# Performance work log

Measured on AMD Instinct MI355X. Metric: run time of the kernel, lower is better.

The kernel has to match this reference:

```python
import jax, jax.numpy as jnp
import numpy as np

THETA = 10000.0
N_HEADS = 16


def setup_inputs() -> dict:
    key = jax.random.key(0)
    kx, kq, kk, kv, ko = jax.random.split(key, 5)
    B, S, D = 2, 2048, 1024
    std = np.sqrt(2.0 / (D + D))
    def mk_w(k):
        # trunc_normal in [-3*std, 3*std], stored as [in_features, out_features]
        return jax.random.truncated_normal(k, -3.0, 3.0, (D, D), jnp.float32) * std
    return {
        "x": jax.random.normal(kx, (B, S, D), dtype=jnp.float32),
        "token_positions": jnp.arange(S, dtype=jnp.int64) if jax.config.jax_enable_x64 else jnp.arange(S, dtype=jnp.int32),
        "WQ": mk_w(kq),
        "WK": mk_w(kk),
        "WV": mk_w(kv),
        "WO": mk_w(ko),
    }


def _rope(x, pos, theta):
    # x: [B, H, S, d_k]; pos: [S]
    d_k = x.shape[-1]
    freq = 1.0 / theta ** (jnp.arange(0, d_k, 2, dtype=jnp.float32) / d_k)  # [d_k//2]
    ang = pos.astype(jnp.float32)[:, None] * freq                            # [S, d_k//2]
    cos, sin = jnp.cos(ang), jnp.sin(ang)
    xp = x.reshape(x.shape[:-1] + (d_k // 2, 2))
    x0, x1 = xp[..., 0], xp[..., 1]
    r0 = cos * x0 - sin * x1
    r1 = sin * x0 + cos * x1
    return jnp.stack([r0, r1], axis=-1).reshape(x.shape)


def reference(x, token_positions, WQ, WK, WV, WO):
    B, S, D = x.shape
    H = N_HEADS
    dk = D // H
    # Linear in source computes y = x @ W.T (W stored [in, out], used transposed)
    def proj(W):
        return jnp.einsum('oi,bsi->bso', W, x).reshape(B, S, H, dk).transpose(0, 2, 1, 3)
    Q = proj(WQ)  # [B, H, S, dk]
    K = proj(WK)
    V = proj(WV)
    Q = _rope(Q, token_positions, THETA)
    K = _rope(K, token_positions, THETA)
    scores = jnp.einsum('bhqd,bhkd->bhqk', Q, K) / np.sqrt(dk).astype(np.float32)
    causal = jnp.tril(jnp.ones((S, S), dtype=bool))
    scores = jnp.where(causal, scores, jnp.float32(-1e9))
    w = jax.nn.softmax(scores, axis=-1)
    out = jnp.einsum('bhqk,bhkd->bhqd', w, V)
    out = out.transpose(0, 2, 1, 3).reshape(B, S, D)
    return jnp.einsum('oi,bsi->bso', WO, out)
```

## Files before the change

kernel.cpp:

```cpp
#include <hip/hip_runtime.h>
#include <hip/hip_bf16.h>

#define S_LEN   2048
#define D_MODEL 1024
#define NH      16
#define DKH     64
#define BATCH   2
#define BS_ROWS 4096

typedef unsigned short u16;
typedef unsigned int   u32;
typedef __attribute__((ext_vector_type(4)))  float f32x4;
typedef __attribute__((ext_vector_type(16))) float f32x16;
typedef __attribute__((ext_vector_type(8)))  short bf16x8;

__device__ __forceinline__ float bf2f(u16 u) {
  union { unsigned int i; float f; } v; v.i = ((unsigned int)u) << 16; return v.f;
}
__device__ __forceinline__ u16 f2bf(float f) {
  union { __hip_bfloat16 h; u16 u; } cv; cv.h = __float2bfloat16(f); return cv.u;
}
__device__ __forceinline__ u32 pkbf(float a, float b) {
  return (u32)f2bf(a) | ((u32)f2bf(b) << 16);
}
__device__ __forceinline__ f32x4 mfma16(bf16x8 a, bf16x8 b, f32x4 c) {
  return __builtin_amdgcn_mfma_f32_16x16x32_bf16(a, b, c, 0, 0, 0);
}
__device__ __forceinline__ f32x16 mfma32(bf16x8 a, bf16x8 b, f32x16 c) {
  return __builtin_amdgcn_mfma_f32_32x32x16_bf16(a, b, c, 0, 0, 0);
}
__device__ __forceinline__ void gl_lds16(const u16* g, u16* l) {
  __builtin_amdgcn_global_load_lds(
      (const __attribute__((address_space(1))) void*)g,
      (__attribute__((address_space(3))) void*)l, 16, 0, 0);
}

__global__ void cvt_all(const float* __restrict__ x,
                        const float* __restrict__ wq, const float* __restrict__ wk,
                        const float* __restrict__ wv, const float* __restrict__ wo,
                        u16* __restrict__ xb, u16* __restrict__ wqb, u16* __restrict__ wkb,
                        u16* __restrict__ wvb, u16* __restrict__ wob) {
  int seg = blockIdx.y;
  const float* src; u16* dst;
  if (seg < 4)      { src = x + (size_t)seg * (1u << 20); dst = xb + (size_t)seg * (1u << 20); }
  else if (seg == 4){ src = wq; dst = wqb; }
  else if (seg == 5){ src = wk; dst = wkb; }
  else if (seg == 6){ src = wv; dst = wvb; }
  else              { src = wo; dst = wob; }
  int i = blockIdx.x * 256 + threadIdx.x;
  float4 v = reinterpret_cast<const float4*>(src)[i];
  ushort4 o;
  o.x = f2bf(v.x); o.y = f2bf(v.y); o.z = f2bf(v.z); o.w = f2bf(v.w);
  reinterpret_cast<ushort4*>(dst)[i] = o;
}

#define BM 128
#define BN 128
#define BKK 64

__global__ __launch_bounds__(256) void gemm_bt(
    const u16* __restrict__ A,
    const u16* __restrict__ B0, const u16* __restrict__ B1, const u16* __restrict__ B2,
    u16* __restrict__ C0, u16* __restrict__ C1, u16* __restrict__ C2,
    float* __restrict__ Cf,
    int M, int N, int K, int out_f32)
{
  __shared__ __align__(16) u16 As[BM * BKK];
  __shared__ __align__(16) u16 Bs[BN * BKK];

  const int z = blockIdx.z;
  const u16* Bm = (z == 0) ? B0 : ((z == 1) ? B1 : B2);
  u16* Cb = (z == 0) ? C0 : ((z == 1) ? C1 : C2);

  const int tid = threadIdx.x;
  const int l = tid & 63, w = tid >> 6;
  const int lr = l & 15, lg = l >> 4;
  const int m0 = blockIdx.y * BM, n0 = blockIdx.x * BN;
  const int wr = w >> 1, wc = w & 1;

  f32x4 acc[4][4];
#pragma unroll
  for (int mi = 0; mi < 4; ++mi)
#pragma unroll
    for (int nj = 0; nj < 4; ++nj)
      acc[mi][nj] = (f32x4){0.f, 0.f, 0.f, 0.f};

  for (int k0 = 0; k0 < K; k0 += BKK) {
    __syncthreads();
#pragma unroll
    for (int i = 0; i < 4; ++i) {
      int Dc = w * 256 + i * 64 + l;
      int row = Dc >> 3;
      int c = (Dc & 7) ^ (row & 7);
      gl_lds16(A  + (size_t)(m0 + row) * K + k0 + c * 8, As + (w * 256 + i * 64) * 8);
      gl_lds16(Bm + (size_t)(n0 + row) * K + k0 + c * 8, Bs + (w * 256 + i * 64) * 8);
    }
    __syncthreads();

    bf16x8 af[2][4], bfr[2][4];
#pragma unroll
    for (int kk = 0; kk < 2; ++kk)
#pragma unroll
      for (int mi = 0; mi < 4; ++mi) {
        int rowa = wr * 64 + mi * 16 + lr;
        int ck = kk * 4 + lg;
        af[kk][mi] = *(const bf16x8*)&As[rowa * BKK + (((ck) ^ (rowa & 7)) << 3)];
        int rowb = wc * 64 + mi * 16 + lr;
        bfr[kk][mi] = *(const bf16x8*)&Bs[rowb * BKK + (((ck) ^ (rowb & 7)) << 3)];
      }
#pragma unroll
    for (int kk = 0; kk < 2; ++kk)
#pragma unroll
      for (int mi = 0; mi < 4; ++mi)
#pragma unroll
        for (int nj = 0; nj < 4; ++nj)
          acc[mi][nj] = mfma16(af[kk][mi], bfr[kk][nj], acc[mi][nj]);
  }

#pragma unroll
  for (int mi = 0; mi < 4; ++mi)
#pragma unroll
    for (int nj = 0; nj < 4; ++nj)
#pragma unroll
      for (int r = 0; r < 4; ++r) {
        int row = m0 + wr * 64 + mi * 16 + lg * 4 + r;
        int col = n0 + wc * 64 + nj * 16 + lr;
        float v = acc[mi][nj][r];
        if (out_f32) Cf[(size_t)row * N + col] = v;
        else         Cb[(size_t)row * N + col] = f2bf(v);
      }
}

__global__ void rope_pack(const u16* __restrict__ Yq, const u16* __restrict__ Yk,
                          const int* __restrict__ pos,
                          u16* __restrict__ Qb, u16* __restrict__ Kb)
{
  int t = blockIdx.x * blockDim.x + threadIdx.x;
  if (t >= BS_ROWS * (D_MODEL / 2)) return;
  int pi = t & 511;
  int r  = t >> 9;
  int h = pi >> 5, j = pi & 31;
  int b = r >> 11, s = r & (S_LEN - 1);
  int p = pos[s];

  float freq = exp2f(-(float)j * 0.41524101186092028f);
  float ang = (float)p * freq;
  float sn, cs;
  sincosf(ang, &sn, &cs);

  int base = r * D_MODEL + pi * 2;
  float q0 = bf2f(Yq[base]), q1 = bf2f(Yq[base + 1]);
  float k0 = bf2f(Yk[base]), k1 = bf2f(Yk[base + 1]);

  const float QS = 0.18033688011112042f;
  float qr0 = (cs * q0 - sn * q1) * QS;
  float qr1 = (sn * q0 + cs * q1) * QS;
  float kr0 = cs * k0 - sn * k1;
  float kr1 = sn * k0 + cs * k1;

  int bh = b * NH + h;
  size_t qidx = ((size_t)bh * S_LEN + s) * DKH + 2 * j;
  ushort2 qo; qo.x = f2bf(qr0); qo.y = f2bf(qr1);
  ushort2 ko; ko.x = f2bf(kr0); ko.y = f2bf(kr1);
  *reinterpret_cast<ushort2*>(Qb + qidx) = qo;
  *reinterpret_cast<ushort2*>(Kb + qidx) = ko;
}

__global__ __launch_bounds__(256) void transpose_v(const u16* __restrict__ Yv,
                                                   u16* __restrict__ Vt)
{
  __shared__ u32 T[64][65];
  const int sb = blockIdx.x;
  const int bh = blockIdx.y;
  const int b = bh >> 4, h = bh & 15;
  const int t = threadIdx.x;
  const int s0 = sb * 64;

#pragma unroll
  for (int pass = 0; pass < 2; ++pass) {
    int row = pass * 32 + (t >> 3);
    int c0 = (t & 7) * 8;
    bf16x8 v = *(const bf16x8*)(Yv + (size_t)(b * S_LEN + s0 + row) * D_MODEL + h * DKH + c0);
#pragma unroll
    for (int i = 0; i < 8; ++i) T[row][c0 + i] = (u32)(u16)v[i];
  }
  __syncthreads();

  const int d = t >> 2, ch = t & 3;
  bf16x8 o0, o1;
#pragma unroll
  for (int i = 0; i < 8; ++i) o0[i] = (short)(u16)T[ch * 16 + i][d];
#pragma unroll
  for (int i = 0; i < 8; ++i) o1[i] = (short)(u16)T[ch * 16 + 8 + i][d];
  u16* dst = Vt + ((size_t)bh * DKH + d) * S_LEN + s0 + ch * 16;
  *(bf16x8*)dst = o0;
  *(bf16x8*)(dst + 8) = o1;
}

__global__ __launch_bounds__(256, 2) void attn_fwd(
    const u16* __restrict__ Qb, const u16* __restrict__ Kb,
    const u16* __restrict__ Vt, u16* __restrict__ Ob)
{
  const int f = blockIdx.x;
  const int qt = (f < 256) ? (f >> 5) : (23 - (f >> 5));
  const int bh = f & 31;
  const int b = bh >> 4, h = bh & 15;
  const int tid = threadIdx.x, l = tid & 63, w = tid >> 6;
  const int lq = l & 31;
  const int hi = l >> 5;

  __shared__ __align__(16) u16 Ks[2][64 * 64];
  __shared__ __align__(16) u16 Vs[2][64 * 64];

  const u16* Qh = Qb + (size_t)bh * S_LEN * DKH;
  const u16* Kh = Kb + (size_t)bh * S_LEN * DKH;
  const u16* Vh = Vt + (size_t)bh * DKH * S_LEN;

  const int q0w = qt * 128 + w * 32;
  const int qg  = q0w + lq;

  bf16x8 qf[4];
#pragma unroll
  for (int ks = 0; ks < 4; ++ks)
    qf[ks] = *(const bf16x8*)(Qh + (size_t)qg * DKH + ks * 16 + hi * 8);

  f32x16 oacc[2];
#pragma unroll
  for (int r = 0; r < 16; ++r) { oacc[0][r] = 0.f; oacc[1][r] = 0.f; }
  float m = -INFINITY, lsum = 0.f;

#define STAGE(buf, tt) do {                                                        \
    int kv0s = (tt) * 64;                                                          \
    _Pragma("unroll")                                                              \
    for (int i = 0; i < 2; ++i) {                                                  \
      int Dc = w * 128 + i * 64 + l;                                               \
      int row = Dc >> 3;                                                           \
      int c = (Dc & 7) ^ (row & 7);                                                \
      gl_lds16(Kh + (size_t)(kv0s + row) * DKH + c * 8, &Ks[buf][(w * 128 + i * 64) * 8]); \
      gl_lds16(Vh + (size_t)row * S_LEN + kv0s + c * 8, &Vs[buf][(w * 128 + i * 64) * 8]); \
    }                                                                              \
  } while (0)

  const int nt = 2 * qt + 2;
  STAGE(0, 0);
  __syncthreads();
  int cur = 0;
  for (int t = 0; t < nt; ++t) {
    if (t + 1 < nt) STAGE(cur ^ 1, t + 1);
    const int kv0 = t * 64;
    if (kv0 <= q0w + 31) {
      f32x16 sv0, sv1;
#pragma unroll
      for (int r = 0; r < 16; ++r) { sv0[r] = 0.f; sv1[r] = 0.f; }
#pragma unroll
      for (int ks = 0; ks < 4; ++ks) {
        int c0 = ((ks * 2 + hi) ^ (l & 7)) << 3;
        bf16x8 k0 = *(const bf16x8*)&Ks[cur][lq * 64 + c0];
        bf16x8 k1 = *(const bf16x8*)&Ks[cur][(32 + lq) * 64 + c0];
        sv0 = mfma32(k0, qf[ks], sv0);
        sv1 = mfma32(k1, qf[ks], sv1);
      }
      if (kv0 + 63 > q0w) {
#pragma unroll
        for (int r = 0; r < 16; ++r) {
          int kvl = (r & 3) + 8 * (r >> 2) + 4 * hi;
          if (kv0 + kvl > qg)      sv0[r] = -1e30f;
          if (kv0 + 32 + kvl > qg) sv1[r] = -1e30f;
        }
      }
      float pm = sv0[0];
#pragma unroll
      for (int r = 1; r < 16; ++r) pm = fmaxf(pm, sv0[r]);
#pragma unroll
      for (int r = 0; r < 16; ++r) pm = fmaxf(pm, sv1[r]);
      pm = fmaxf(pm, __shfl_xor(pm, 32));
      if (__any(pm > m + 8.f)) {
        float mn = fmaxf(m, pm);
        float sc = exp2f(m - mn);
        m = mn; lsum *= sc;
#pragma unroll
        for (int r = 0; r < 16; ++r) {
          float sr = __shfl(sc, (r & 3) + 8 * (r >> 2) + 4 * hi);
          oacc[0][r] *= sr; oacc[1][r] *= sr;
        }
      }
      float ps = 0.f;
#pragma unroll
      for (int r = 0; r < 16; ++r) { float p = exp2f(sv0[r] - m); sv0[r] = p; ps += p; }
#pragma unroll
      for (int r = 0; r < 16; ++r) { float p = exp2f(sv1[r] - m); sv1[r] = p; ps += p; }
      lsum += ps;
#pragma unroll
      for (int s = 0; s < 2; ++s) {
        u32 w0[4], w1[4];
#pragma unroll
        for (int g = 0; g < 4; ++g) {
          float a0 = s ? sv1[4 * g]     : sv0[4 * g];
          float a1 = s ? sv1[4 * g + 1] : sv0[4 * g + 1];
          float a2 = s ? sv1[4 * g + 2] : sv0[4 * g + 2];
          float a3 = s ? sv1[4 * g + 3] : sv0[4 * g + 3];
          w0[g] = pkbf(a0, a1);
          w1[g] = pkbf(a2, a3);
        }
#pragma unroll
        for (int t2 = 0; t2 < 2; ++t2) {
          u32 xo0 = hi ? w0[2 * t2 + 1] : w0[2 * t2];
          u32 xo1 = hi ? w1[2 * t2 + 1] : w1[2 * t2];
          u32 sp0 = hi ? w0[2 * t2]     : w0[2 * t2 + 1];
          u32 sp1 = hi ? w1[2 * t2]     : w1[2 * t2 + 1];
          u32 yo0 = __shfl_xor(sp0, 32);
          u32 yo1 = __shfl_xor(sp1, 32);
          union { u32 u[4]; bf16x8 v; } pa;
          pa.u[0] = hi ? yo0 : xo0;
          pa.u[1] = hi ? yo1 : xo1;
          pa.u[2] = hi ? xo0 : yo0;
          pa.u[3] = hi ? xo1 : yo1;
          int ks2 = s * 2 + t2;
          int cv = ((ks2 * 2 + hi) ^ (l & 7)) << 3;
#pragma unroll
          for (int dh = 0; dh < 2; ++dh) {
            bf16x8 vf = *(const bf16x8*)&Vs[cur][(dh * 32 + lq) * 64 + cv];
            oacc[dh] = mfma32(pa.v, vf, oacc[dh]);
          }
        }
      }
    }
    __syncthreads();
    cur ^= 1;
  }
#undef STAGE

  float ltot = lsum + __shfl_xor(lsum, 32);
  float inv = 1.0f / ltot;
  u16* obase = Ob + (size_t)b * S_LEN * D_MODEL + (size_t)h * DKH;
#pragma unroll
  for (int r = 0; r < 16; ++r) {
    int ql = (r & 3) + 8 * (r >> 2) + 4 * hi;
    float ir = __shfl(inv, ql);
    u16* orow = obase + (size_t)(q0w + ql) * D_MODEL;
    orow[lq]      = f2bf(oacc[0][r] * ir);
    orow[32 + lq] = f2bf(oacc[1][r] * ir);
  }
}

extern "C" void kernel_launch(void* const* d_in, const int* in_sizes, int n_in,
                              void* d_out, int out_size, void* d_ws, size_t ws_size,
                              hipStream_t stream) {
  const float* x   = (const float*)d_in[0];
  const int*   pos = (const int*)d_in[1];
  const float* WQ  = (const float*)d_in[2];
  const float* WK  = (const float*)d_in[3];
  const float* WV  = (const float*)d_in[4];
  const float* WO  = (const float*)d_in[5];

  char* ws = (char*)d_ws;
  u16* xb  = (u16*)(ws);
  u16* wqb = (u16*)(ws + (size_t)(8)  * 1048576);
  u16* wkb = (u16*)(ws + (size_t)(10) * 1048576);
  u16* wvb = (u16*)(ws + (size_t)(12) * 1048576);
  u16* wob = (u16*)(ws + (size_t)(14) * 1048576);
  u16* Yq  = (u16*)(ws + (size_t)(16) * 1048576);
  u16* Yk  = (u16*)(ws + (size_t)(24) * 1048576);
  u16* Yv  = (u16*)(ws + (size_t)(32) * 1048576);
  u16* Qb  = (u16*)(ws + (size_t)(40) * 1048576);
  u16* Kb  = (u16*)(ws + (size_t)(48) * 1048576);
  u16* Vt  = (u16*)(ws + (size_t)(56) * 1048576);
  u16* Ob  = (u16*)(ws + (size_t)(64) * 1048576);

  cvt_all<<<dim3(1024, 8), 256, 0, stream>>>(x, WQ, WK, WV, WO, xb, wqb, wkb, wvb, wob);

  gemm_bt<<<dim3(D_MODEL / BN, BS_ROWS / BM, 3), 256, 0, stream>>>(
      xb, wqb, wkb, wvb, Yq, Yk, Yv, nullptr, BS_ROWS, D_MODEL, D_MODEL, 0);

  rope_pack<<<(BS_ROWS * (D_MODEL / 2)) / 256, 256, 0, stream>>>(
      Yq, Yk, pos, Qb, Kb);

  transpose_v<<<dim3(S_LEN / 64, BATCH * NH), 256, 0, stream>>>(Yv, Vt);

  attn_fwd<<<dim3(512), 256, 0, stream>>>(Qb, Kb, Vt, Ob);

  gemm_bt<<<dim3(D_MODEL / BN, BS_ROWS / BM, 1), 256, 0, stream>>>(
      Ob, wob, wob, wob, nullptr, nullptr, nullptr, (float*)d_out,
      BS_ROWS, D_MODEL, D_MODEL, 1);
}
```

Measured before the change: 226.9 us.

## Restructure attention into single-wave blocks with 32-row KV tiles

The attention kernel moves from 256-thread blocks handling 128 query rows to 64-thread single-wave blocks handling 32 query rows, launched as 2048 blocks in longest-first order. KV tiles shrink to 32 rows with their own swizzle, the causal masking becomes exact per tile, and __syncthreads is replaced by a vmcnt wait because only one wave touches shared memory. The aim is finer-grained parallelism, better load balance across the causal triangle and no block-level barriers. In exchange, each block reuses K/V less, so global/L2 traffic for K and V grows, and each wave does more loads per MFMA.

```diff
diff --git a/kernel.cpp b/kernel.cpp
--- a/kernel.cpp
+++ b/kernel.cpp
@@ -197,138 +197,132 @@
   *(bf16x8*)(dst + 8) = o1;
 }
 
-__global__ __launch_bounds__(256, 2) void attn_fwd(
+__global__ __launch_bounds__(64) void attn_fwd(
     const u16* __restrict__ Qb, const u16* __restrict__ Kb,
     const u16* __restrict__ Vt, u16* __restrict__ Ob)
 {
   const int f = blockIdx.x;
-  const int qt = (f < 256) ? (f >> 5) : (23 - (f >> 5));
+  const int qt = 63 - (f >> 5);
   const int bh = f & 31;
   const int b = bh >> 4, h = bh & 15;
-  const int tid = threadIdx.x, l = tid & 63, w = tid >> 6;
-  const int lq = l & 31;
-  const int hi = l >> 5;
-
-  __shared__ __align__(16) u16 Ks[2][64 * 64];
-  __shared__ __align__(16) u16 Vs[2][64 * 64];
+  const int l = threadIdx.x & 63;
+  const int lq = l & 31, hi = l >> 5;
+
+  __shared__ __align__(16) u16 Ks[2][32 * 64];
+  __shared__ __align__(16) u16 Vs[2][64 * 32];
 
   const u16* Qh = Qb + (size_t)bh * S_LEN * DKH;
   const u16* Kh = Kb + (size_t)bh * S_LEN * DKH;
   const u16* Vh = Vt + (size_t)bh * DKH * S_LEN;
 
-  const int q0w = qt * 128 + w * 32;
-  const int qg  = q0w + lq;
+  const int q0 = qt * 32;
 
   bf16x8 qf[4];
 #pragma unroll
   for (int ks = 0; ks < 4; ++ks)
-    qf[ks] = *(const bf16x8*)(Qh + (size_t)qg * DKH + ks * 16 + hi * 8);
+    qf[ks] = *(const bf16x8*)(Qh + (size_t)(q0 + lq) * DKH + ks * 16 + hi * 8);
+
+  const u16* ksrc[4];
+  const u16* vsrc[4];
+#pragma unroll
+  for (int i = 0; i < 4; ++i) {
+    int Dc = i * 64 + l;
+    int row = Dc >> 3;
+    int c = (Dc & 7) ^ (row & 7);
+    ksrc[i] = Kh + (size_t)row * DKH + c * 8;
+  }
+#pragma unroll
+  for (int i = 0; i < 4; ++i) {
+    int Dc = i * 64 + l;
+    int d = Dc >> 2;
+    int c = (Dc & 3) ^ (d & 3);
+    vsrc[i] = Vh + (size_t)d * S_LEN + c * 8;
+  }
 
   f32x16 oacc[2];
 #pragma unroll
   for (int r = 0; r < 16; ++r) { oacc[0][r] = 0.f; oacc[1][r] = 0.f; }
   float m = -INFINITY, lsum = 0.f;
 
-#define STAGE(buf, tt) do {                                                        \
-    int kv0s = (tt) * 64;                                                          \
-    _Pragma("unroll")                                                              \
-    for (int i = 0; i < 2; ++i) {                                                  \
-      int Dc = w * 128 + i * 64 + l;                                               \
-      int row = Dc >> 3;                                                           \
-      int c = (Dc & 7) ^ (row & 7);                                                \
-      gl_lds16(Kh + (size_t)(kv0s + row) * DKH + c * 8, &Ks[buf][(w * 128 + i * 64) * 8]); \
-      gl_lds16(Vh + (size_t)row * S_LEN + kv0s + c * 8, &Vs[buf][(w * 128 + i * 64) * 8]); \
-    }                                                                              \
-  } while (0)
-
-  const int nt = 2 * qt + 2;
-  STAGE(0, 0);
-  __syncthreads();
+  auto stage = [&](int buf, int t) {
+    const size_t koff = (size_t)t * 32 * DKH;
+    const size_t voff = (size_t)t * 32;
+#pragma unroll
+    for (int i = 0; i < 4; ++i) gl_lds16(ksrc[i] + koff, &Ks[buf][i * 512]);
+#pragma unroll
+    for (int i = 0; i < 4; ++i) gl_lds16(vsrc[i] + voff, &Vs[buf][i * 512]);
+  };
+
+  const int nt = qt + 1;
+  stage(0, 0);
   int cur = 0;
   for (int t = 0; t < nt; ++t) {
-    if (t + 1 < nt) STAGE(cur ^ 1, t + 1);
-    const int kv0 = t * 64;
-    if (kv0 <= q0w + 31) {
-      f32x16 sv0, sv1;
-#pragma unroll
-      for (int r = 0; r < 16; ++r) { sv0[r] = 0.f; sv1[r] = 0.f; }
-#pragma unroll
-      for (int ks = 0; ks < 4; ++ks) {
-        int c0 = ((ks * 2 + hi) ^ (l & 7)) << 3;
-        bf16x8 k0 = *(const bf16x8*)&Ks[cur][lq * 64 + c0];
-        bf16x8 k1 = *(const bf16x8*)&Ks[cur][(32 + lq) * 64 + c0];
-        sv0 = mfma32(k0, qf[ks], sv0);
-        sv1 = mfma32(k1, qf[ks], sv1);
-      }
-      if (kv0 + 63 > q0w) {
-#pragma unroll
-        for (int r = 0; r < 16; ++r) {
-          int kvl = (r & 3) + 8 * (r >> 2) + 4 * hi;
-          if (kv0 + kvl > qg)      sv0[r] = -1e30f;
-          if (kv0 + 32 + kvl > qg) sv1[r] = -1e30f;
-        }
-      }
-      float pm = sv0[0];
-#pragma unroll
-      for (int r = 1; r < 16; ++r) pm = fmaxf(pm, sv0[r]);
-#pragma unroll
-      for (int r = 0; r < 16; ++r) pm = fmaxf(pm, sv1[r]);
-      pm = fmaxf(pm, __shfl_xor(pm, 32));
-      if (__any(pm > m + 8.f)) {
-        float mn = fmaxf(m, pm);
-        float sc = exp2f(m - mn);
-        m = mn; lsum *= sc;
-#pragma unroll
-        for (int r = 0; r < 16; ++r) {
-          float sr = __shfl(sc, (r & 3) + 8 * (r >> 2) + 4 * hi);
-          oacc[0][r] *= sr; oacc[1][r] *= sr;
-        }
-      }
-      float ps = 0.f;
-#pragma unroll
-      for (int r = 0; r < 16; ++r) { float p = exp2f(sv0[r] - m); sv0[r] = p; ps += p; }
-#pragma unroll
-      for (int r = 0; r < 16; ++r) { float p = exp2f(sv1[r] - m); sv1[r] = p; ps += p; }
-      lsum += ps;
-#pragma unroll
-      for (int s = 0; s < 2; ++s) {
-        u32 w0[4], w1[4];
-#pragma unroll
-        for (int g = 0; g < 4; ++g) {
-          float a0 = s ? sv1[4 * g]     : sv0[4 * g];
-          float a1 = s ? sv1[4 * g + 1] : sv0[4 * g + 1];
-          float a2 = s ? sv1[4 * g + 2] : sv0[4 * g + 2];
-          float a3 = s ? sv1[4 * g + 3] : sv0[4 * g + 3];
-          w0[g] = pkbf(a0, a1);
-          w1[g] = pkbf(a2, a3);
-        }
-#pragma unroll
-        for (int t2 = 0; t2 < 2; ++t2) {
-          u32 xo0 = hi ? w0[2 * t2 + 1] : w0[2 * t2];
-          u32 xo1 = hi ? w1[2 * t2 + 1] : w1[2 * t2];
-          u32 sp0 = hi ? w0[2 * t2]     : w0[2 * t2 + 1];
-          u32 sp1 = hi ? w1[2 * t2]     : w1[2 * t2 + 1];
-          u32 yo0 = __shfl_xor(sp0, 32);
-          u32 yo1 = __shfl_xor(sp1, 32);
-          union { u32 u[4]; bf16x8 v; } pa;
-          pa.u[0] = hi ? yo0 : xo0;
-          pa.u[1] = hi ? yo1 : xo1;
-          pa.u[2] = hi ? xo0 : yo0;
-          pa.u[3] = hi ? xo1 : yo1;
-          int ks2 = s * 2 + t2;
-          int cv = ((ks2 * 2 + hi) ^ (l & 7)) << 3;
-#pragma unroll
-          for (int dh = 0; dh < 2; ++dh) {
-            bf16x8 vf = *(const bf16x8*)&Vs[cur][(dh * 32 + lq) * 64 + cv];
-            oacc[dh] = mfma32(pa.v, vf, oacc[dh]);
-          }
-        }
-      }
-    }
-    __syncthreads();
+    asm volatile("s_waitcnt vmcnt(0)" ::: "memory");
+    __builtin_amdgcn_sched_barrier(0);
+    if (t + 1 < nt) stage(cur ^ 1, t + 1);
+
+    f32x16 sv;
+#pragma unroll
+    for (int r = 0; r < 16; ++r) sv[r] = 0.f;
+#pragma unroll
+    for (int ks = 0; ks < 4; ++ks) {
+      int c0 = ((ks * 2 + hi) ^ (lq & 7)) << 3;
+      bf16x8 kf = *(const bf16x8*)&Ks[cur][lq * 64 + c0];
+      sv = mfma32(kf, qf[ks], sv);
+    }
+    if (t == qt) {
+#pragma unroll
+      for (int r = 0; r < 16; ++r) {
+        int kvl = (r & 3) + 8 * (r >> 2) + 4 * hi;
+        if (kvl > lq) sv[r] = -1e30f;
+      }
+    }
+    float pm = sv[0];
+#pragma unroll
+    for (int r = 1; r < 16; ++r) pm = fmaxf(pm, sv[r]);
+    pm = fmaxf(pm, __shfl_xor(pm, 32));
+    if (__any(pm > m + 8.f)) {
+      float mn = fmaxf(m, pm);
+      float sc = exp2f(m - mn);
+      m = mn; lsum *= sc;
+#pragma unroll
+      for (int r = 0; r < 16; ++r) {
+        float sr = __shfl(sc, (r & 3) + 8 * (r >> 2) + 4 * hi);
+        oacc[0][r] *= sr; oacc[1][r] *= sr;
+      }
+    }
+    float ps = 0.f;
+#pragma unroll
+    for (int r = 0; r < 16; ++r) { float p = exp2f(sv[r] - m); sv[r] = p; ps += p; }
+    lsum += ps;
+    u32 w0[4], w1[4];
+#pragma unroll
+    for (int g = 0; g < 4; ++g) {
+      w0[g] = pkbf(sv[4 * g],     sv[4 * g + 1]);
+      w1[g] = pkbf(sv[4 * g + 2], sv[4 * g + 3]);
+    }
+#pragma unroll
+    for (int t2 = 0; t2 < 2; ++t2) {
+      u32 xo0 = hi ? w0[2 * t2 + 1] : w0[2 * t2];
+      u32 xo1 = hi ? w1[2 * t2 + 1] : w1[2 * t2];
+      u32 sp0 = hi ? w0[2 * t2]     : w0[2 * t2 + 1];
+      u32 sp1 = hi ? w1[2 * t2]     : w1[2 * t2 + 1];
+      u32 yo0 = __shfl_xor(sp0, 32);
+      u32 yo1 = __shfl_xor(sp1, 32);
+      union { u32 u[4]; bf16x8 v; } pa;
+      pa.u[0] = hi ? yo0 : xo0;
+      pa.u[1] = hi ? yo1 : xo1;
+      pa.u[2] = hi ? xo0 : yo0;
+      pa.u[3] = hi ? xo1 : yo1;
+      int cv = ((t2 * 2 + hi) ^ (lq & 3)) << 3;
+#pragma unroll
+      for (int dh = 0; dh < 2; ++dh) {
+        bf16x8 vf = *(const bf16x8*)&Vs[cur][(dh * 32 + lq) * 32 + cv];
+        oacc[dh] = mfma32(pa.v, vf, oacc[dh]);
+      }
+    }
     cur ^= 1;
   }
-#undef STAGE
 
   float ltot = lsum + __shfl_xor(lsum, 32);
   float inv = 1.0f / ltot;
@@ -337,7 +331,7 @@
   for (int r = 0; r < 16; ++r) {
     int ql = (r & 3) + 8 * (r >> 2) + 4 * hi;
     float ir = __shfl(inv, ql);
-    u16* orow = obase + (size_t)(q0w + ql) * D_MODEL;
+    u16* orow = obase + (size_t)(q0 + ql) * D_MODEL;
     orow[lq]      = f2bf(oacc[0][r] * ir);
     orow[32 + lq] = f2bf(oacc[1][r] * ir);
   }
@@ -377,7 +371,7 @@
 
   transpose_v<<<dim3(S_LEN / 64, BATCH * NH), 256, 0, stream>>>(Yv, Vt);
 
-  attn_fwd<<<dim3(512), 256, 0, stream>>>(Qb, Kb, Vt, Ob);
+  attn_fwd<<<dim3(2048), 64, 0, stream>>>(Qb, Kb, Vt, Ob);
 
   gemm_bt<<<dim3(D_MODEL / BN, BS_ROWS / BM, 1), 256, 0, stream>>>(
       Ob, wob, wob, wob, nullptr, nullptr, nullptr, (float*)d_out,
```

New measurement: 245.6 us. 8.2% more time.
